# Kernel optimization log

Measured on AMD Instinct MI355X. Metric: run time of the kernel, lower is better.

The kernel has to match this reference:

```python
import jax, jax.numpy as jnp
import numpy as np

N_RAYS, N_SAMPLES, RES = 4096, 256, 128
RGB_C = 15
XYZ_MIN, XYZ_MAX = -1.0, 1.0
NEAR, FAR, STEPSIZE, BG = 0.2, 3.0, 0.5, 1.0
ALPHA_INIT = 0.01
ACT_SHIFT = float(np.log(1.0 / (1.0 - ALPHA_INIT) - 1.0))
N_FREQ = 6
EMB_DIM = 3 + 3 * 2 * N_FREQ  # 39
DIM0 = RGB_C + EMB_DIM        # 54


def _trilinear(grid, u):
    # grid: [C, R, R, R]; u: [N, 3] normalized to [0,1]; align_corners=True
    R = grid.shape[1]
    pos = jnp.clip(u, 0.0, 1.0) * (R - 1)
    i0 = jnp.clip(jnp.floor(pos).astype(jnp.int32), 0, R - 2)
    f = pos - i0.astype(pos.dtype)
    i1 = i0 + 1
    x0, y0, z0 = i0[:, 0], i0[:, 1], i0[:, 2]
    x1, y1, z1 = i1[:, 0], i1[:, 1], i1[:, 2]
    fx, fy, fz = f[:, 0], f[:, 1], f[:, 2]
    c = (grid[:, x0, y0, z0] * ((1 - fx) * (1 - fy) * (1 - fz))
         + grid[:, x1, y0, z0] * (fx * (1 - fy) * (1 - fz))
         + grid[:, x0, y1, z0] * ((1 - fx) * fy * (1 - fz))
         + grid[:, x0, y0, z1] * ((1 - fx) * (1 - fy) * fz)
         + grid[:, x1, y1, z0] * (fx * fy * (1 - fz))
         + grid[:, x1, y0, z1] * (fx * (1 - fy) * fz)
         + grid[:, x0, y1, z1] * ((1 - fx) * fy * fz)
         + grid[:, x1, y1, z1] * (fx * fy * fz))
    return c.T  # [N, C]


def _embed(x):
    # NeRF positional encoding, multires=6, include inputs: [..., 3] -> [..., 39]
    freqs = 2.0 ** jnp.arange(N_FREQ, dtype=x.dtype)
    xb = x[..., None, :] * freqs[:, None]  # [..., 6, 3]
    shp = x.shape[:-1]
    return jnp.concatenate([x, jnp.sin(xb).reshape(*shp, -1), jnp.cos(xb).reshape(*shp, -1)], -1)


def setup_inputs() -> dict:
    key = jax.random.key(0)
    ks = jax.random.split(key, 12)
    return {
        "rays_o": jax.random.uniform(ks[0], (N_RAYS, 3), minval=-0.5, maxval=0.5),
        "rays_d": jax.random.normal(ks[1], (N_RAYS, 3)),
        "viewdirs": jax.random.normal(ks[2], (N_RAYS, 3)),
        "latent_grid": jax.random.normal(ks[3], (1 + RGB_C, RES, RES, RES)) * 0.1,
        "normals_grid": jax.random.normal(ks[4], (3, RES, RES, RES)),
        "W0": jax.random.normal(ks[5], (DIM0, 64)) * 0.1, "b0": jnp.zeros((64,)),
        "W1": jax.random.normal(ks[6], (64, 64)) * 0.1, "b1": jnp.zeros((64,)),
        "W2": jax.random.normal(ks[7], (64, 64)) * 0.1, "b2": jnp.zeros((64,)),
        "W3": jax.random.normal(ks[8], (64, 3)) * 0.1, "b3": jnp.zeros((3,)),
    }


def reference(rays_o, rays_d, viewdirs, latent_grid, normals_grid,
              W0, b0, W1, b1, W2, b2, W3, b3):
    rays_d = rays_d / jnp.linalg.norm(rays_d, axis=-1, keepdims=True)
    viewdirs = viewdirs / jnp.linalg.norm(viewdirs, axis=-1, keepdims=True)
    # sample_ray: uniform steps along each ray
    t = jnp.linspace(NEAR, FAR, N_SAMPLES, dtype=rays_o.dtype)
    ray_pts = rays_o[:, None, :] + rays_d[:, None, :] * t[None, :, None]  # [R,S,3]
    inbbox = jnp.all((ray_pts >= XYZ_MIN) & (ray_pts <= XYZ_MAX), -1)      # [R,S]
    u = ((ray_pts - XYZ_MIN) / (XYZ_MAX - XYZ_MIN)).reshape(-1, 3)
    lat = _trilinear(latent_grid, u).reshape(N_RAYS, N_SAMPLES, 1 + RGB_C)
    nrm = _trilinear(normals_grid, u).reshape(N_RAYS, N_SAMPLES, 3)
    nrm = nrm / jnp.maximum(jnp.linalg.norm(nrm, axis=-1, keepdims=True), 1e-12)
    nrm = jnp.where(inbbox[..., None], nrm, 0.0)
    density = lat[..., 0]
    # activate_density: 1 - exp(-softplus(d + shift) * interval), zero outside bbox
    alpha = jnp.where(inbbox, 1.0 - jnp.exp(-jax.nn.softplus(density + ACT_SHIFT) * STEPSIZE), 0.0)
    # cumprod_exclusive transmittance
    alphainv_cum = jnp.concatenate(
        [jnp.ones_like(alpha[..., :1]), jnp.cumprod(jnp.clip(1.0 - alpha, 1e-10, None), -1)], -1)
    weights = alpha * alphainv_cum[..., :-1]
    # reflection directions: 2*(-v.n)*n + v
    vde = jnp.broadcast_to(viewdirs[:, None, :], nrm.shape)
    dot = jnp.sum(-vde * nrm, -1, keepdims=True)
    refdirs = 2.0 * dot * nrm + vde
    feat = jnp.concatenate([jnp.where(inbbox[..., None], lat[..., 1:], 0.0), _embed(refdirs)], -1)
    h = jax.nn.relu(feat @ W0 + b0)
    h = jax.nn.relu(h @ W1 + b1)
    h = jax.nn.relu(h @ W2 + b2)
    rgb = jnp.where(inbbox[..., None], jax.nn.sigmoid(h @ W3 + b3), 0.0)
    rgb_marched = jnp.sum(weights[..., None] * rgb, -2) + alphainv_cum[..., -1:] * BG
    depth = jnp.linalg.norm(rays_o[:, None, :] - ray_pts, axis=-1)
    depth_marched = jnp.sum(weights * depth, -1) + alphainv_cum[..., -1] * FAR
    disp = 1.0 / depth_marched
    acc = weights.sum(-1)
    normals_marched = jnp.sum(weights[..., None] * nrm, -2)
    return rgb_marched, depth_marched, disp, acc, normals_marched, weights, alphainv_cum
```

## Files before the change

### kernel.cpp

```cpp
#include <hip/hip_runtime.h>
#include <hip/hip_bf16.h>
#include <math.h>

typedef __hip_bfloat16 bf16;
typedef float f32x4 __attribute__((ext_vector_type(4)));
typedef float f32x2 __attribute__((ext_vector_type(2)));
typedef short short8 __attribute__((ext_vector_type(8)));
typedef short short4v __attribute__((ext_vector_type(4)));

#define NRAYS 4096
#define NSAMP 256
#define RESG  128
#define RS2   16384
#define RS3   2097152
#define ACT_SHIFT (-4.59511985013459f)

#define OFLAG 0
#define OBIAS 16
#define ORO   272
#define ORD   12560
#define OVD   24848
#define FRAG_BYTE_OFF 148544
#define LATIL_BYTE_OFF 1048576ULL
#define NRMIL_BYTE_OFF 68157440ULL
#define WS_NEED        101711872ULL

__device__ __forceinline__ float ldT(const float* p, size_t i){ return p[i]; }
__device__ __forceinline__ float ldT(const bf16*  p, size_t i){ return __bfloat162float(p[i]); }

__device__ __forceinline__ unsigned short f2bu(float f){
  unsigned int x = __float_as_uint(f);
  unsigned int r = (x + 0x7FFFu + ((x >> 16) & 1u)) >> 16;
  return (unsigned short)r;
}
__device__ __forceinline__ float bu2f(short s){
  return __uint_as_float(((unsigned int)(unsigned short)s) << 16);
}

#define PREP_BLOCKS 53

template<typename T>
__device__ void fill_ws_part(const void* W0,const void* b0,const void* W1,const void* b1,
                             const void* W2,const void* b2,const void* W3,const void* b3,
                             const void* ro,const void* rd,const void* vd,
                             float* __restrict__ wb, int bid, int tid, bool isf32)
{
  const T* tW0=(const T*)W0; const T* tb0=(const T*)b0;
  const T* tW1=(const T*)W1; const T* tb1=(const T*)b1;
  const T* tW2=(const T*)W2; const T* tb2=(const T*)b2;
  const T* tW3=(const T*)W3; const T* tb3=(const T*)b3;
  const T* tro=(const T*)ro; const T* trd=(const T*)rd; const T* tvd=(const T*)vd;

  unsigned short* fu = (unsigned short*)((char*)wb + FRAG_BYTE_OFF);

  if (bid < 16){
    const int r = bid*256 + tid;
    float ox = ldT(tro, r*3+0), oy = ldT(tro, r*3+1), oz = ldT(tro, r*3+2);
    wb[ORO+r*3+0]=ox; wb[ORO+r*3+1]=oy; wb[ORO+r*3+2]=oz;
    float dx = ldT(trd, r*3+0), dy = ldT(trd, r*3+1), dz = ldT(trd, r*3+2);
    float dn = 1.0f / sqrtf(dx*dx+dy*dy+dz*dz);
    wb[ORD+r*3+0]=dx*dn; wb[ORD+r*3+1]=dy*dn; wb[ORD+r*3+2]=dz*dn;
    float vx = ldT(tvd, r*3+0), vy = ldT(tvd, r*3+1), vz = ldT(tvd, r*3+2);
    float vn = 1.0f / sqrtf(vx*vx+vy*vy+vz*vz);
    wb[OVD+r*3+0]=vx*vn; wb[OVD+r*3+1]=vy*vn; wb[OVD+r*3+2]=vz*vn;
  } else if (bid < 32){
    const int idx = (bid-16)*256 + tid;
    int blk = idx >> 9, rem = idx & 511, lane = rem >> 3, j = rem & 7;
    int nt = blk >> 1, ks = blk & 1;
    int k = ks*32 + ((lane>>4)<<3) + j, n = nt*16 + (lane & 15);
    float v = (k < 54) ? ldT(tW0, k*64 + n) : 0.0f;
    fu[idx] = f2bu(v);
  } else if (bid < 48){
    const int idx = (bid-32)*256 + tid;
    int blk = idx >> 9, rem = idx & 511, lane = rem >> 3, j = rem & 7;
    int nt = blk >> 1, ks = blk & 1;
    int k = ks*32 + ((lane>>4)<<3) + j, n = nt*16 + (lane & 15);
    fu[4096+idx] = f2bu(ldT(tW1, k*64 + n));
    fu[8192+idx] = f2bu(ldT(tW2, k*64 + n));
  } else if (bid < 52){
    const int idx = (bid-48)*256 + tid;
    int blk = idx >> 9, rem = idx & 511, lane = rem >> 3, j = rem & 7;
    int ks = blk;
    int k = ks*32 + ((lane>>4)<<3) + j, n = lane & 15;
    float v = (n < 3) ? ldT(tW3, k*3 + n) : 0.0f;
    fu[12288+idx] = f2bu(v);
  } else {
    if (tid < 64){
      wb[16+tid]  = ldT(tb0, tid);
      wb[80+tid]  = ldT(tb1, tid);
      wb[144+tid] = ldT(tb2, tid);
    }
    if (tid < 16) wb[224+tid] = (tid < 3) ? ldT(tb3, tid) : 0.0f;
    if (tid == 0) wb[OFLAG] = isf32 ? 1.0f : 0.0f;
  }
}

__global__ __launch_bounds__(256)
void prep(const void* W0,const void* b0,const void* W1,const void* b1,
          const void* W2,const void* b2,const void* W3,const void* b3,
          const void* ro,const void* rd,const void* vd,
          float* __restrict__ wb)
{
  __shared__ int s_f32;
  const int tid = threadIdx.x;
  const int bid = blockIdx.x;
  if (tid == 0) s_f32 = 0;
  __syncthreads();
  {
    const bf16* t1 = (const bf16*)W1;
    float a = fabsf(__bfloat162float(t1[2*tid]));
    float b = fabsf(__bfloat162float(t1[2*tid+1]));
    if (!(a < 100.0f) || !(b < 100.0f)) atomicOr(&s_f32, 1);
  }
  __syncthreads();
  const bool isf32 = (s_f32 != 0);
  if (isf32) fill_ws_part<float>(W0,b0,W1,b1,W2,b2,W3,b3,ro,rd,vd,wb,bid,tid,true);
  else       fill_ws_part<bf16 >(W0,b0,W1,b1,W2,b2,W3,b3,ro,rd,vd,wb,bid,tid,false);
}

#define IL_BLOCKS 6144

__global__ __launch_bounds__(256)
void interleave_all(const void* __restrict__ latent, const void* __restrict__ normals,
                    float* __restrict__ wb)
{
  const bool isf32 = (wb[OFLAG] > 0.5f);
  const int bid = blockIdx.x;
  if (bid < 4096){
    unsigned short* lat_il = (unsigned short*)((char*)wb + LATIL_BYTE_OFF);
    const int v0 = (bid*256 + (int)threadIdx.x) * 2;
    short8 o0a, o0b, o1a, o1b;
    if (isf32){
      const float* p = (const float*)latent;
#pragma unroll
      for (int c = 0; c < 8; c++){
        f32x2 r0 = *(const f32x2*)&p[(size_t)c*RS3 + v0];
        o0a[c] = (short)f2bu(r0[0]); o1a[c] = (short)f2bu(r0[1]);
        f32x2 r1 = *(const f32x2*)&p[(size_t)(c+8)*RS3 + v0];
        o0b[c] = (short)f2bu(r1[0]); o1b[c] = (short)f2bu(r1[1]);
      }
    } else {
      const unsigned short* p = (const unsigned short*)latent;
#pragma unroll
      for (int c = 0; c < 8; c++){
        unsigned int r0 = *(const unsigned int*)&p[(size_t)c*RS3 + v0];
        o0a[c] = (short)(r0 & 0xFFFFu); o1a[c] = (short)(r0 >> 16);
        unsigned int r1 = *(const unsigned int*)&p[(size_t)(c+8)*RS3 + v0];
        o0b[c] = (short)(r1 & 0xFFFFu); o1b[c] = (short)(r1 >> 16);
      }
    }
    unsigned short* q = &lat_il[(size_t)v0 << 4];
    *(short8*)&q[0]  = o0a;
    *(short8*)&q[8]  = o0b;
    *(short8*)&q[16] = o1a;
    *(short8*)&q[24] = o1b;
  } else {
    f32x4* nrm_il = (f32x4*)((char*)wb + NRMIL_BYTE_OFF);
    const int v0 = ((bid-4096)*256 + (int)threadIdx.x) * 4;
    f32x4 a, b, c;
    if (isf32){
      const float* p = (const float*)normals;
      a = *(const f32x4*)&p[v0];
      b = *(const f32x4*)&p[(size_t)RS3 + v0];
      c = *(const f32x4*)&p[(size_t)2*RS3 + v0];
    } else {
      const unsigned short* p = (const unsigned short*)normals;
      short4v sa = *(const short4v*)&p[v0];
      short4v sb = *(const short4v*)&p[(size_t)RS3 + v0];
      short4v sc = *(const short4v*)&p[(size_t)2*RS3 + v0];
      a = (f32x4){bu2f(sa[0]), bu2f(sa[1]), bu2f(sa[2]), bu2f(sa[3])};
      b = (f32x4){bu2f(sb[0]), bu2f(sb[1]), bu2f(sb[2]), bu2f(sb[3])};
      c = (f32x4){bu2f(sc[0]), bu2f(sc[1]), bu2f(sc[2]), bu2f(sc[3])};
    }
#pragma unroll
    for (int j = 0; j < 4; j++){
      nrm_il[v0 + j] = (f32x4){a[j], b[j], c[j], 0.0f};
    }
  }
}

__global__ __launch_bounds__(256, 4)
void render_fast(const float* __restrict__ wb, float* __restrict__ out)
{
  const int ray  = blockIdx.x;
  const int i    = threadIdx.x;
  const int lane = i & 63;
  const int wv   = i >> 6;
  const int quad = lane >> 4;
  const int n15  = lane & 15;
  const int wbase = wv * 64;

  __shared__ unsigned short act[NSAMP*72];
  __shared__ float sh_w[NSAMP];
  __shared__ float sh_wt[4];
  __shared__ float red[4][8];
  __shared__ float red_rgb[4][16];

  const unsigned short* lat_il = (const unsigned short*)((const char*)wb + LATIL_BYTE_OFF);
  const f32x4* nrm_il = (const f32x4*)((const char*)wb + NRMIL_BYTE_OFF);

  const float ox = wb[ORO+ray*3+0], oy = wb[ORO+ray*3+1], oz = wb[ORO+ray*3+2];
  const float dx = wb[ORD+ray*3+0], dy = wb[ORD+ray*3+1], dz = wb[ORD+ray*3+2];
  const float vx = wb[OVD+ray*3+0], vy = wb[OVD+ray*3+1], vz = wb[OVD+ray*3+2];

  const float t  = 0.2f + (2.8f/255.0f) * (float)i;
  const float px = ox + dx*t, py = oy + dy*t, pz = oz + dz*t;
  const bool inb = (px >= -1.0f) & (px <= 1.0f) & (py >= -1.0f) & (py <= 1.0f)
                 & (pz >= -1.0f) & (pz <= 1.0f);

  float alpha = 0.0f, nx = 0.0f, ny = 0.0f, nz = 0.0f;
  unsigned short* arow = &act[i*72];

  if (inb) {
    float ux = fminf(fmaxf((px+1.0f)*0.5f, 0.0f), 1.0f) * 127.0f;
    float uy = fminf(fmaxf((py+1.0f)*0.5f, 0.0f), 1.0f) * 127.0f;
    float uz = fminf(fmaxf((pz+1.0f)*0.5f, 0.0f), 1.0f) * 127.0f;
    int x0 = (int)floorf(ux); x0 = x0 > 126 ? 126 : (x0 < 0 ? 0 : x0);
    int y0 = (int)floorf(uy); y0 = y0 > 126 ? 126 : (y0 < 0 ? 0 : y0);
    int z0 = (int)floorf(uz); z0 = z0 > 126 ? 126 : (z0 < 0 ? 0 : z0);
    float fx = ux - (float)x0, fy = uy - (float)y0, fz = uz - (float)z0;
    const float gx = 1.0f - fx, gy = 1.0f - fy, gz = 1.0f - fz;

    const int vb = (x0<<14) + (y0<<7) + z0;
    const unsigned short* Lp = lat_il + ((size_t)vb<<4);
    const f32x4* Np = nrm_il + vb;

    float ch[16];
#pragma unroll
    for (int c = 0; c < 16; c++) ch[c] = 0.0f;
    float nr0 = 0.0f, nr1 = 0.0f, nr2 = 0.0f;

    const int   loff[4] = {0, 1<<18, 1<<11, (1<<18)+(1<<11)};
    const int   noff[4] = {0, 16384, 128, 16384+128};
    const float wxy[4]  = {gx*gy, fx*gy, gx*fy, fx*fy};

#pragma unroll
    for (int cr = 0; cr < 4; cr++){
      const unsigned short* p = Lp + loff[cr];
      short8 a0 = *(const short8*)(p);
      short8 a1 = *(const short8*)(p+8);
      short8 b0 = *(const short8*)(p+16);
      short8 b1 = *(const short8*)(p+24);
      const float wz0 = wxy[cr]*gz, wz1 = wxy[cr]*fz;
#pragma unroll
      for (int j = 0; j < 8; j++){
        ch[j]   += wz0*bu2f(a0[j]) + wz1*bu2f(b0[j]);
        ch[j+8] += wz0*bu2f(a1[j]) + wz1*bu2f(b1[j]);
      }
      f32x4 n0 = Np[noff[cr]];
      f32x4 n1 = Np[noff[cr]+1];
      nr0 += wz0*n0[0] + wz1*n1[0];
      nr1 += wz0*n0[1] + wz1*n1[1];
      nr2 += wz0*n0[2] + wz1*n1[2];
    }

    float xs = ch[0] + ACT_SHIFT;
    float sp = xs > 15.0f ? xs : log1pf(__expf(xs));
    alpha = 1.0f - __expf(-sp * 0.5f);

    float nn  = sqrtf(nr0*nr0 + nr1*nr1 + nr2*nr2);
    float ninv = 1.0f / fmaxf(nn, 1e-12f);
    nx = nr0*ninv; ny = nr1*ninv; nz = nr2*ninv;

    float dt = -(vx*nx + vy*ny + vz*nz);
    float rx = 2.0f*dt*nx + vx, ry = 2.0f*dt*ny + vy, rz = 2.0f*dt*nz + vz;

    short8 v0, v1;
#pragma unroll
    for (int j = 0; j < 8; j++) v0[j] = (short)f2bu(ch[1+j]);
#pragma unroll
    for (int j = 0; j < 7; j++) v1[j] = (short)f2bu(ch[9+j]);
    v1[7] = (short)f2bu(rx);
    *(short8*)&arow[0] = v0; *(short8*)&arow[8] = v1;
    v0[0]=(short)f2bu(ry); v0[1]=(short)f2bu(rz);
    v0[2]=(short)f2bu(__sinf(rx));        v0[3]=(short)f2bu(__sinf(ry));        v0[4]=(short)f2bu(__sinf(rz));
    v0[5]=(short)f2bu(__sinf(rx*2.0f));   v0[6]=(short)f2bu(__sinf(ry*2.0f));   v0[7]=(short)f2bu(__sinf(rz*2.0f));
    v1[0]=(short)f2bu(__sinf(rx*4.0f));   v1[1]=(short)f2bu(__sinf(ry*4.0f));   v1[2]=(short)f2bu(__sinf(rz*4.0f));
    v1[3]=(short)f2bu(__sinf(rx*8.0f));   v1[4]=(short)f2bu(__sinf(ry*8.0f));   v1[5]=(short)f2bu(__sinf(rz*8.0f));
    v1[6]=(short)f2bu(__sinf(rx*16.0f));  v1[7]=(short)f2bu(__sinf(ry*16.0f));
    *(short8*)&arow[16] = v0; *(short8*)&arow[24] = v1;
    v0[0]=(short)f2bu(__sinf(rz*16.0f));  v0[1]=(short)f2bu(__sinf(rx*32.0f));
    v0[2]=(short)f2bu(__sinf(ry*32.0f));  v0[3]=(short)f2bu(__sinf(rz*32.0f));
    v0[4]=(short)f2bu(__cosf(rx));        v0[5]=(short)f2bu(__cosf(ry));        v0[6]=(short)f2bu(__cosf(rz));
    v0[7]=(short)f2bu(__cosf(rx*2.0f));
    v1[0]=(short)f2bu(__cosf(ry*2.0f));   v1[1]=(short)f2bu(__cosf(rz*2.0f));
    v1[2]=(short)f2bu(__cosf(rx*4.0f));   v1[3]=(short)f2bu(__cosf(ry*4.0f));   v1[4]=(short)f2bu(__cosf(rz*4.0f));
    v1[5]=(short)f2bu(__cosf(rx*8.0f));   v1[6]=(short)f2bu(__cosf(ry*8.0f));   v1[7]=(short)f2bu(__cosf(rz*8.0f));
    *(short8*)&arow[32] = v0; *(short8*)&arow[40] = v1;
    v0[0]=(short)f2bu(__cosf(rx*16.0f));  v0[1]=(short)f2bu(__cosf(ry*16.0f));  v0[2]=(short)f2bu(__cosf(rz*16.0f));
    v0[3]=(short)f2bu(__cosf(rx*32.0f));  v0[4]=(short)f2bu(__cosf(ry*32.0f));  v0[5]=(short)f2bu(__cosf(rz*32.0f));
    v0[6]=0; v0[7]=0;
#pragma unroll
    for (int j = 0; j < 8; j++) v1[j] = 0;
    *(short8*)&arow[48] = v0; *(short8*)&arow[56] = v1;
  } else {
    short8 z;
#pragma unroll
    for (int j = 0; j < 8; j++) z[j] = 0;
#pragma unroll
    for (int c = 0; c < 8; c++) *(short8*)&arow[c*8] = z;
  }

  float xv = fmaxf(1.0f - alpha, 1e-10f);
  float incl = xv;
#pragma unroll
  for (int off = 1; off < 64; off <<= 1){
    float y = __shfl_up(incl, off, 64);
    if (lane >= off) incl *= y;
  }
  float excl = __shfl_up(incl, 1, 64);
  if (lane == 0) excl = 1.0f;
  if (lane == 63) sh_wt[wv] = incl;
  __syncthreads();

  float pre = 1.0f;
#pragma unroll
  for (int k = 0; k < 4; k++) if (k < wv) pre *= sh_wt[k];
  const float last = sh_wt[0]*sh_wt[1]*sh_wt[2]*sh_wt[3];
  const float av = pre * excl;
  const float w  = alpha * av;
  sh_w[i] = w;

  float* outw = out + 36864;
  float* outa = out + 36864 + 1048576;
  outw[ray*NSAMP + i] = w;
  outa[ray*(NSAMP+1) + i] = av;
  if (i == NSAMP-1) outa[ray*(NSAMP+1) + NSAMP] = last;

  {
    float vals[5] = { w*t, w, w*nx, w*ny, w*nz };
#pragma unroll
    for (int v = 0; v < 5; v++){
      float s = vals[v];
#pragma unroll
      for (int m = 32; m > 0; m >>= 1) s += __shfl_xor(s, m, 64);
      if (lane == 0) red[wv][v] = s;
    }
  }
  __syncthreads();
  if (i == 0){
    float s0 = red[0][0]+red[1][0]+red[2][0]+red[3][0];
    float s1 = red[0][1]+red[1][1]+red[2][1]+red[3][1];
    float s2 = red[0][2]+red[1][2]+red[2][2]+red[3][2];
    float s3 = red[0][3]+red[1][3]+red[2][3]+red[3][3];
    float s4 = red[0][4]+red[1][4]+red[2][4]+red[3][4];
    const float dm = s0 + last * 3.0f;
    float* o1 = out + 12288; o1[ray] = dm;
    float* o2 = out + 16384; o2[ray] = 1.0f / dm;
    float* o3 = out + 20480; o3[ray] = s1;
    float* o4 = out + 24576;
    o4[ray*3+0] = s2; o4[ray*3+1] = s3; o4[ray*3+2] = s4;
  }

  const short8* fr = (const short8*)((const char*)wb + FRAG_BYTE_OFF);

#pragma unroll
  for (int l = 0; l < 3; l++){
    const int fbase = l * 512;
    f32x4 acc[4][4];
#pragma unroll
    for (int mt = 0; mt < 4; mt++)
#pragma unroll
      for (int nt = 0; nt < 4; nt++) acc[mt][nt] = (f32x4){0.f,0.f,0.f,0.f};

#pragma unroll
    for (int ks = 0; ks < 2; ks++){
      short8 a[4], b[4];
#pragma unroll
      for (int mt = 0; mt < 4; mt++)
        a[mt] = *(const short8*)&act[(wbase + mt*16 + n15)*72 + ks*32 + quad*8];
#pragma unroll
      for (int nt = 0; nt < 4; nt++)
        b[nt] = fr[fbase + (nt*2+ks)*64 + lane];
#pragma unroll
      for (int mt = 0; mt < 4; mt++)
#pragma unroll
        for (int nt = 0; nt < 4; nt++)
          acc[mt][nt] = __builtin_amdgcn_mfma_f32_16x16x32_bf16(a[mt], b[nt], acc[mt][nt], 0, 0, 0);
    }
    __syncthreads();
#pragma unroll
    for (int nt = 0; nt < 4; nt++){
      const float bn = wb[OBIAS + l*64 + nt*16 + n15];
#pragma unroll
      for (int mt = 0; mt < 4; mt++){
#pragma unroll
        for (int r = 0; r < 4; r++){
          float vv = fmaxf(acc[mt][nt][r] + bn, 0.0f);
          act[(wbase + mt*16 + quad*4 + r)*72 + nt*16 + n15] = f2bu(vv);
        }
      }
    }
    __syncthreads();
  }

  {
    f32x4 acc3[4];
#pragma unroll
    for (int mt = 0; mt < 4; mt++) acc3[mt] = (f32x4){0.f,0.f,0.f,0.f};
#pragma unroll
    for (int ks = 0; ks < 2; ks++){
      short8 a[4];
#pragma unroll
      for (int mt = 0; mt < 4; mt++)
        a[mt] = *(const short8*)&act[(wbase + mt*16 + n15)*72 + ks*32 + quad*8];
      short8 b = fr[1536 + ks*64 + lane];
#pragma unroll
      for (int mt = 0; mt < 4; mt++)
        acc3[mt] = __builtin_amdgcn_mfma_f32_16x16x32_bf16(a[mt], b, acc3[mt], 0, 0, 0);
    }
    const float bn3 = wb[OBIAS + 208 + n15];
    float p = 0.0f;
#pragma unroll
    for (int mt = 0; mt < 4; mt++){
#pragma unroll
      for (int r = 0; r < 4; r++){
        const float wr = sh_w[wbase + mt*16 + quad*4 + r];
        const float logit = acc3[mt][r] + bn3;
        p += wr * (1.0f / (1.0f + __expf(-logit)));
      }
    }
    p += __shfl_xor(p, 16, 64);
    p += __shfl_xor(p, 32, 64);
    if (lane < 16) red_rgb[wv][lane] = p;
  }
  __syncthreads();
  if (i < 3){
    float s = red_rgb[0][i] + red_rgb[1][i] + red_rgb[2][i] + red_rgb[3][i];
    out[ray*3+i] = s + last;
  }
}

template<typename GT>
__device__ __forceinline__ void render_body(const GT* __restrict__ latent,
                                            const GT* __restrict__ normals,
                                            const float* __restrict__ wb,
                                            float* __restrict__ out)
{
  const int ray  = blockIdx.x;
  const int i    = threadIdx.x;
  const int lane = i & 63;
  const int wv   = i >> 6;
  const int quad = lane >> 4;
  const int n15  = lane & 15;
  const int wbase = wv * 64;

  __shared__ unsigned short act[NSAMP*72];
  __shared__ float sh_w[NSAMP];
  __shared__ float sh_wt[4];
  __shared__ float red[4][8];
  __shared__ float red_rgb[4][16];

  const float ox = wb[ORO+ray*3+0], oy = wb[ORO+ray*3+1], oz = wb[ORO+ray*3+2];
  const float dx = wb[ORD+ray*3+0], dy = wb[ORD+ray*3+1], dz = wb[ORD+ray*3+2];
  const float vx = wb[OVD+ray*3+0], vy = wb[OVD+ray*3+1], vz = wb[OVD+ray*3+2];

  const float t  = 0.2f + (2.8f/255.0f) * (float)i;
  const float px = ox + dx*t, py = oy + dy*t, pz = oz + dz*t;
  const bool inb = (px >= -1.0f) & (px <= 1.0f) & (py >= -1.0f) & (py <= 1.0f)
                 & (pz >= -1.0f) & (pz <= 1.0f);

  float alpha = 0.0f, nx = 0.0f, ny = 0.0f, nz = 0.0f;
  float fv[64];
#pragma unroll
  for (int k = 0; k < 64; k++) fv[k] = 0.0f;

  if (inb) {
    float ux = fminf(fmaxf((px+1.0f)*0.5f, 0.0f), 1.0f) * 127.0f;
    float uy = fminf(fmaxf((py+1.0f)*0.5f, 0.0f), 1.0f) * 127.0f;
    float uz = fminf(fmaxf((pz+1.0f)*0.5f, 0.0f), 1.0f) * 127.0f;
    int x0 = (int)floorf(ux); x0 = x0 > 126 ? 126 : (x0 < 0 ? 0 : x0);
    int y0 = (int)floorf(uy); y0 = y0 > 126 ? 126 : (y0 < 0 ? 0 : y0);
    int z0 = (int)floorf(uz); z0 = z0 > 126 ? 126 : (z0 < 0 ? 0 : z0);
    float fx = ux - (float)x0, fy = uy - (float)y0, fz = uz - (float)z0;
    const int base = x0*RS2 + y0*RESG + z0;
    const float gx = 1.0f - fx, gy = 1.0f - fy, gz = 1.0f - fz;
    const float w000 = gx*gy*gz, w100 = fx*gy*gz, w010 = gx*fy*gz, w001 = gx*gy*fz;
    const float w110 = fx*fy*gz, w101 = fx*gy*fz, w011 = gx*fy*fz, w111 = fx*fy*fz;

    float ch[19];
#pragma unroll
    for (int c = 0; c < 19; c++){
      const GT* g = (c < 16 ? latent + c*RS3 : normals + (c-16)*RS3) + base;
      ch[c] = w000*ldT(g,0)        + w100*ldT(g,RS2)
            + w010*ldT(g,RESG)     + w001*ldT(g,1)
            + w110*ldT(g,RS2+RESG) + w101*ldT(g,RS2+1)
            + w011*ldT(g,RESG+1)   + w111*ldT(g,RS2+RESG+1);
    }

    float xs = ch[0] + ACT_SHIFT;
    float sp = xs > 15.0f ? xs : log1pf(__expf(xs));
    alpha = 1.0f - __expf(-sp * 0.5f);

    float nn  = sqrtf(ch[16]*ch[16] + ch[17]*ch[17] + ch[18]*ch[18]);
    float ninv = 1.0f / fmaxf(nn, 1e-12f);
    nx = ch[16]*ninv; ny = ch[17]*ninv; nz = ch[18]*ninv;

    float dt = -(vx*nx + vy*ny + vz*nz);
    float rx = 2.0f*dt*nx + vx, ry = 2.0f*dt*ny + vy, rz = 2.0f*dt*nz + vz;

#pragma unroll
    for (int k = 0; k < 15; k++) fv[k] = ch[k+1];
    fv[15] = rx; fv[16] = ry; fv[17] = rz;
#pragma unroll
    for (int f = 0; f < 6; f++){
      float s = (float)(1 << f);
      fv[18 + f*3 + 0] = __sinf(rx*s);
      fv[18 + f*3 + 1] = __sinf(ry*s);
      fv[18 + f*3 + 2] = __sinf(rz*s);
      fv[36 + f*3 + 0] = __cosf(rx*s);
      fv[36 + f*3 + 1] = __cosf(ry*s);
      fv[36 + f*3 + 2] = __cosf(rz*s);
    }
  }

#pragma unroll
  for (int c = 0; c < 8; c++){
    short8 v;
#pragma unroll
    for (int k = 0; k < 8; k++) v[k] = (short)f2bu(fv[c*8+k]);
    *(short8*)&act[i*72 + c*8] = v;
  }

  float xvv = fmaxf(1.0f - alpha, 1e-10f);
  float incl = xvv;
#pragma unroll
  for (int off = 1; off < 64; off <<= 1){
    float y = __shfl_up(incl, off, 64);
    if (lane >= off) incl *= y;
  }
  float excl = __shfl_up(incl, 1, 64);
  if (lane == 0) excl = 1.0f;
  if (lane == 63) sh_wt[wv] = incl;
  __syncthreads();

  float pre = 1.0f;
#pragma unroll
  for (int k = 0; k < 4; k++) if (k < wv) pre *= sh_wt[k];
  const float last = sh_wt[0]*sh_wt[1]*sh_wt[2]*sh_wt[3];
  const float av = pre * excl;
  const float w  = alpha * av;
  sh_w[i] = w;

  float* outw = out + 36864;
  float* outa = out + 36864 + 1048576;
  outw[ray*NSAMP + i] = w;
  outa[ray*(NSAMP+1) + i] = av;
  if (i == NSAMP-1) outa[ray*(NSAMP+1) + NSAMP] = last;

  {
    float vals[5] = { w*t, w, w*nx, w*ny, w*nz };
#pragma unroll
    for (int v = 0; v < 5; v++){
      float s = vals[v];
#pragma unroll
      for (int m = 32; m > 0; m >>= 1) s += __shfl_xor(s, m, 64);
      if (lane == 0) red[wv][v] = s;
    }
  }
  __syncthreads();
  if (i == 0){
    float s0 = red[0][0]+red[1][0]+red[2][0]+red[3][0];
    float s1 = red[0][1]+red[1][1]+red[2][1]+red[3][1];
    float s2 = red[0][2]+red[1][2]+red[2][2]+red[3][2];
    float s3 = red[0][3]+red[1][3]+red[2][3]+red[3][3];
    float s4 = red[0][4]+red[1][4]+red[2][4]+red[3][4];
    const float dm = s0 + last * 3.0f;
    float* o1 = out + 12288; o1[ray] = dm;
    float* o2 = out + 16384; o2[ray] = 1.0f / dm;
    float* o3 = out + 20480; o3[ray] = s1;
    float* o4 = out + 24576;
    o4[ray*3+0] = s2; o4[ray*3+1] = s3; o4[ray*3+2] = s4;
  }

  const short8* fr = (const short8*)((const char*)wb + FRAG_BYTE_OFF);

#pragma unroll
  for (int l = 0; l < 3; l++){
    const int fbase = l * 512;
    f32x4 acc[4][4];
#pragma unroll
    for (int mt = 0; mt < 4; mt++)
#pragma unroll
      for (int nt = 0; nt < 4; nt++) acc[mt][nt] = (f32x4){0.f,0.f,0.f,0.f};

#pragma unroll
    for (int ks = 0; ks < 2; ks++){
      short8 a[4], b[4];
#pragma unroll
      for (int mt = 0; mt < 4; mt++)
        a[mt] = *(const short8*)&act[(wbase + mt*16 + n15)*72 + ks*32 + quad*8];
#pragma unroll
      for (int nt = 0; nt < 4; nt++)
        b[nt] = fr[fbase + (nt*2+ks)*64 + lane];
#pragma unroll
      for (int mt = 0; mt < 4; mt++)
#pragma unroll
        for (int nt = 0; nt < 4; nt++)
          acc[mt][nt] = __builtin_amdgcn_mfma_f32_16x16x32_bf16(a[mt], b[nt], acc[mt][nt], 0, 0, 0);
    }
    __syncthreads();
#pragma unroll
    for (int nt = 0; nt < 4; nt++){
      const float bn = wb[OBIAS + l*64 + nt*16 + n15];
#pragma unroll
      for (int mt = 0; mt < 4; mt++){
#pragma unroll
        for (int r = 0; r < 4; r++){
          float vv = fmaxf(acc[mt][nt][r] + bn, 0.0f);
          act[(wbase + mt*16 + quad*4 + r)*72 + nt*16 + n15] = f2bu(vv);
        }
      }
    }
    __syncthreads();
  }

  {
    f32x4 acc3[4];
#pragma unroll
    for (int mt = 0; mt < 4; mt++) acc3[mt] = (f32x4){0.f,0.f,0.f,0.f};
#pragma unroll
    for (int ks = 0; ks < 2; ks++){
      short8 a[4];
#pragma unroll
      for (int mt = 0; mt < 4; mt++)
        a[mt] = *(const short8*)&act[(wbase + mt*16 + n15)*72 + ks*32 + quad*8];
      short8 b = fr[1536 + ks*64 + lane];
#pragma unroll
      for (int mt = 0; mt < 4; mt++)
        acc3[mt] = __builtin_amdgcn_mfma_f32_16x16x32_bf16(a[mt], b, acc3[mt], 0, 0, 0);
    }
    const float bn3 = wb[OBIAS + 208 + n15];
    float p = 0.0f;
#pragma unroll
    for (int mt = 0; mt < 4; mt++){
#pragma unroll
      for (int r = 0; r < 4; r++){
        const float wr = sh_w[wbase + mt*16 + quad*4 + r];
        const float logit = acc3[mt][r] + bn3;
        p += wr * (1.0f / (1.0f + __expf(-logit)));
      }
    }
    p += __shfl_xor(p, 16, 64);
    p += __shfl_xor(p, 32, 64);
    if (lane < 16) red_rgb[wv][lane] = p;
  }
  __syncthreads();
  if (i < 3){
    float s = red_rgb[0][i] + red_rgb[1][i] + red_rgb[2][i] + red_rgb[3][i];
    out[ray*3+i] = s + last;
  }
}

__global__ __launch_bounds__(256)
void render_fallback(const void* __restrict__ latent, const void* __restrict__ normals,
                     const float* __restrict__ wb, float* __restrict__ out)
{
  if (wb[OFLAG] > 0.5f)
    render_body<float>((const float*)latent, (const float*)normals, wb, out);
  else
    render_body<bf16 >((const bf16*)latent,  (const bf16*)normals,  wb, out);
}

extern "C" void kernel_launch(void* const* d_in, const int* in_sizes, int n_in,
                              void* d_out, int out_size, void* d_ws, size_t ws_size,
                              hipStream_t stream)
{
  float* wb = (float*)d_ws;
  prep<<<PREP_BLOCKS, 256, 0, stream>>>(d_in[5], d_in[6], d_in[7], d_in[8],
                                        d_in[9], d_in[10], d_in[11], d_in[12],
                                        d_in[0], d_in[1], d_in[2], wb);
  if (ws_size >= WS_NEED){
    interleave_all<<<IL_BLOCKS, 256, 0, stream>>>(d_in[3], d_in[4], wb);
    render_fast<<<NRAYS, 256, 0, stream>>>(wb, (float*)d_out);
  } else {
    render_fallback<<<NRAYS, 256, 0, stream>>>(d_in[3], d_in[4], wb, (float*)d_out);
  }
}
```

Before: 347.2 us.

## Merge prep and interleave kernels; use packed bf16 converts and sincos

Folds the weight-prep kernel and the grid interleave kernel into one launch. Each block works out the dtype flag locally, so the interleave no longer has to wait on a flag written by an earlier kernel. Float-to-bf16 conversion now uses the v_cvt_pk_bf16_f32 instruction, which converts two values per instruction, in place of manual rounding bit-math. The positional-encoding sin and cos pairs are computed with __sincosf. This removes one kernel launch and cuts ALU work in the per-sample feature build, at the cost of inline asm tied to this GPU architecture and of every block repeating the W1 dtype check.

```diff
diff --git a/kernel.cpp b/kernel.cpp
--- a/kernel.cpp
+++ b/kernel.cpp
@@ -36,6 +36,12 @@
 __device__ __forceinline__ float bu2f(short s){
   return __uint_as_float(((unsigned int)(unsigned short)s) << 16);
 }
+__device__ __forceinline__ unsigned int pkbf(float lo, float hi){
+  unsigned int r;
+  asm("v_cvt_pk_bf16_f32 %0, %1, %2" : "=v"(r) : "v"(lo), "v"(hi));
+  return r;
+}
+union SU { short8 s; unsigned int u[4]; };
 
 #define PREP_BLOCKS 53
 
@@ -95,11 +101,14 @@
   }
 }
 
+#define STAGE_BLOCKS 6208
+
 __global__ __launch_bounds__(256)
-void prep(const void* W0,const void* b0,const void* W1,const void* b1,
-          const void* W2,const void* b2,const void* W3,const void* b3,
-          const void* ro,const void* rd,const void* vd,
-          float* __restrict__ wb)
+void stage(const void* W0,const void* b0,const void* W1,const void* b1,
+           const void* W2,const void* b2,const void* W3,const void* b3,
+           const void* ro,const void* rd,const void* vd,
+           const void* __restrict__ latent, const void* __restrict__ normals,
+           float* __restrict__ wb)
 {
   __shared__ int s_f32;
   const int tid = threadIdx.x;
@@ -114,49 +123,47 @@
   }
   __syncthreads();
   const bool isf32 = (s_f32 != 0);
-  if (isf32) fill_ws_part<float>(W0,b0,W1,b1,W2,b2,W3,b3,ro,rd,vd,wb,bid,tid,true);
-  else       fill_ws_part<bf16 >(W0,b0,W1,b1,W2,b2,W3,b3,ro,rd,vd,wb,bid,tid,false);
-}
-
-#define IL_BLOCKS 6144
-
-__global__ __launch_bounds__(256)
-void interleave_all(const void* __restrict__ latent, const void* __restrict__ normals,
-                    float* __restrict__ wb)
-{
-  const bool isf32 = (wb[OFLAG] > 0.5f);
-  const int bid = blockIdx.x;
-  if (bid < 4096){
+
+  if (bid < 64){
+    if (bid < PREP_BLOCKS){
+      if (isf32) fill_ws_part<float>(W0,b0,W1,b1,W2,b2,W3,b3,ro,rd,vd,wb,bid,tid,true);
+      else       fill_ws_part<bf16 >(W0,b0,W1,b1,W2,b2,W3,b3,ro,rd,vd,wb,bid,tid,false);
+    }
+  } else if (bid < 64 + 4096){
     unsigned short* lat_il = (unsigned short*)((char*)wb + LATIL_BYTE_OFF);
-    const int v0 = (bid*256 + (int)threadIdx.x) * 2;
-    short8 o0a, o0b, o1a, o1b;
+    const int v0 = ((bid-64)*256 + tid) * 2;
+    SU o0a, o0b, o1a, o1b;
     if (isf32){
       const float* p = (const float*)latent;
 #pragma unroll
-      for (int c = 0; c < 8; c++){
-        f32x2 r0 = *(const f32x2*)&p[(size_t)c*RS3 + v0];
-        o0a[c] = (short)f2bu(r0[0]); o1a[c] = (short)f2bu(r0[1]);
-        f32x2 r1 = *(const f32x2*)&p[(size_t)(c+8)*RS3 + v0];
-        o0b[c] = (short)f2bu(r1[0]); o1b[c] = (short)f2bu(r1[1]);
+      for (int c = 0; c < 4; c++){
+        f32x2 ra = *(const f32x2*)&p[(size_t)(2*c  )*RS3 + v0];
+        f32x2 rb = *(const f32x2*)&p[(size_t)(2*c+1)*RS3 + v0];
+        o0a.u[c] = pkbf(ra[0], rb[0]);
+        o1a.u[c] = pkbf(ra[1], rb[1]);
+        f32x2 rc = *(const f32x2*)&p[(size_t)(2*c+8)*RS3 + v0];
+        f32x2 rd2= *(const f32x2*)&p[(size_t)(2*c+9)*RS3 + v0];
+        o0b.u[c] = pkbf(rc[0], rd2[0]);
+        o1b.u[c] = pkbf(rc[1], rd2[1]);
       }
     } else {
       const unsigned short* p = (const unsigned short*)latent;
 #pragma unroll
       for (int c = 0; c < 8; c++){
         unsigned int r0 = *(const unsigned int*)&p[(size_t)c*RS3 + v0];
-        o0a[c] = (short)(r0 & 0xFFFFu); o1a[c] = (short)(r0 >> 16);
+        o0a.s[c] = (short)(r0 & 0xFFFFu); o1a.s[c] = (short)(r0 >> 16);
         unsigned int r1 = *(const unsigned int*)&p[(size_t)(c+8)*RS3 + v0];
-        o0b[c] = (short)(r1 & 0xFFFFu); o1b[c] = (short)(r1 >> 16);
+        o0b.s[c] = (short)(r1 & 0xFFFFu); o1b.s[c] = (short)(r1 >> 16);
       }
     }
     unsigned short* q = &lat_il[(size_t)v0 << 4];
-    *(short8*)&q[0]  = o0a;
-    *(short8*)&q[8]  = o0b;
-    *(short8*)&q[16] = o1a;
-    *(short8*)&q[24] = o1b;
+    *(short8*)&q[0]  = o0a.s;
+    *(short8*)&q[8]  = o0b.s;
+    *(short8*)&q[16] = o1a.s;
+    *(short8*)&q[24] = o1b.s;
   } else {
     f32x4* nrm_il = (f32x4*)((char*)wb + NRMIL_BYTE_OFF);
-    const int v0 = ((bid-4096)*256 + (int)threadIdx.x) * 4;
+    const int v0 = ((bid-4160)*256 + tid) * 4;
     f32x4 a, b, c;
     if (isf32){
       const float* p = (const float*)normals;
@@ -179,6 +186,29 @@
   }
 }
 
+__global__ __launch_bounds__(256)
+void prep(const void* W0,const void* b0,const void* W1,const void* b1,
+          const void* W2,const void* b2,const void* W3,const void* b3,
+          const void* ro,const void* rd,const void* vd,
+          float* __restrict__ wb)
+{
+  __shared__ int s_f32;
+  const int tid = threadIdx.x;
+  const int bid = blockIdx.x;
+  if (tid == 0) s_f32 = 0;
+  __syncthreads();
+  {
+    const bf16* t1 = (const bf16*)W1;
+    float a = fabsf(__bfloat162float(t1[2*tid]));
+    float b = fabsf(__bfloat162float(t1[2*tid+1]));
+    if (!(a < 100.0f) || !(b < 100.0f)) atomicOr(&s_f32, 1);
+  }
+  __syncthreads();
+  const bool isf32 = (s_f32 != 0);
+  if (isf32) fill_ws_part<float>(W0,b0,W1,b1,W2,b2,W3,b3,ro,rd,vd,wb,bid,tid,true);
+  else       fill_ws_part<bf16 >(W0,b0,W1,b1,W2,b2,W3,b3,ro,rd,vd,wb,bid,tid,false);
+}
+
 __global__ __launch_bounds__(256, 4)
 void render_fast(const float* __restrict__ wb, float* __restrict__ out)
 {
@@ -265,34 +295,35 @@
     float dt = -(vx*nx + vy*ny + vz*nz);
     float rx = 2.0f*dt*nx + vx, ry = 2.0f*dt*ny + vy, rz = 2.0f*dt*nz + vz;
 
-    short8 v0, v1;
-#pragma unroll
-    for (int j = 0; j < 8; j++) v0[j] = (short)f2bu(ch[1+j]);
-#pragma unroll
-    for (int j = 0; j < 7; j++) v1[j] = (short)f2bu(ch[9+j]);
-    v1[7] = (short)f2bu(rx);
-    *(short8*)&arow[0] = v0; *(short8*)&arow[8] = v1;
-    v0[0]=(short)f2bu(ry); v0[1]=(short)f2bu(rz);
-    v0[2]=(short)f2bu(__sinf(rx));        v0[3]=(short)f2bu(__sinf(ry));        v0[4]=(short)f2bu(__sinf(rz));
-    v0[5]=(short)f2bu(__sinf(rx*2.0f));   v0[6]=(short)f2bu(__sinf(ry*2.0f));   v0[7]=(short)f2bu(__sinf(rz*2.0f));
-    v1[0]=(short)f2bu(__sinf(rx*4.0f));   v1[1]=(short)f2bu(__sinf(ry*4.0f));   v1[2]=(short)f2bu(__sinf(rz*4.0f));
-    v1[3]=(short)f2bu(__sinf(rx*8.0f));   v1[4]=(short)f2bu(__sinf(ry*8.0f));   v1[5]=(short)f2bu(__sinf(rz*8.0f));
-    v1[6]=(short)f2bu(__sinf(rx*16.0f));  v1[7]=(short)f2bu(__sinf(ry*16.0f));
-    *(short8*)&arow[16] = v0; *(short8*)&arow[24] = v1;
-    v0[0]=(short)f2bu(__sinf(rz*16.0f));  v0[1]=(short)f2bu(__sinf(rx*32.0f));
-    v0[2]=(short)f2bu(__sinf(ry*32.0f));  v0[3]=(short)f2bu(__sinf(rz*32.0f));
-    v0[4]=(short)f2bu(__cosf(rx));        v0[5]=(short)f2bu(__cosf(ry));        v0[6]=(short)f2bu(__cosf(rz));
-    v0[7]=(short)f2bu(__cosf(rx*2.0f));
-    v1[0]=(short)f2bu(__cosf(ry*2.0f));   v1[1]=(short)f2bu(__cosf(rz*2.0f));
-    v1[2]=(short)f2bu(__cosf(rx*4.0f));   v1[3]=(short)f2bu(__cosf(ry*4.0f));   v1[4]=(short)f2bu(__cosf(rz*4.0f));
-    v1[5]=(short)f2bu(__cosf(rx*8.0f));   v1[6]=(short)f2bu(__cosf(ry*8.0f));   v1[7]=(short)f2bu(__cosf(rz*8.0f));
-    *(short8*)&arow[32] = v0; *(short8*)&arow[40] = v1;
-    v0[0]=(short)f2bu(__cosf(rx*16.0f));  v0[1]=(short)f2bu(__cosf(ry*16.0f));  v0[2]=(short)f2bu(__cosf(rz*16.0f));
-    v0[3]=(short)f2bu(__cosf(rx*32.0f));  v0[4]=(short)f2bu(__cosf(ry*32.0f));  v0[5]=(short)f2bu(__cosf(rz*32.0f));
-    v0[6]=0; v0[7]=0;
-#pragma unroll
-    for (int j = 0; j < 8; j++) v1[j] = 0;
-    *(short8*)&arow[48] = v0; *(short8*)&arow[56] = v1;
+    float sX[6], sY[6], sZ[6], cX[6], cY[6], cZ[6];
+#pragma unroll
+    for (int f = 0; f < 6; f++){
+      const float s = (float)(1 << f);
+      __sincosf(rx*s, &sX[f], &cX[f]);
+      __sincosf(ry*s, &sY[f], &cY[f]);
+      __sincosf(rz*s, &sZ[f], &cZ[f]);
+    }
+
+    SU v0, v1;
+    v0.u[0]=pkbf(ch[1],ch[2]);   v0.u[1]=pkbf(ch[3],ch[4]);
+    v0.u[2]=pkbf(ch[5],ch[6]);   v0.u[3]=pkbf(ch[7],ch[8]);
+    v1.u[0]=pkbf(ch[9],ch[10]);  v1.u[1]=pkbf(ch[11],ch[12]);
+    v1.u[2]=pkbf(ch[13],ch[14]); v1.u[3]=pkbf(ch[15],rx);
+    *(short8*)&arow[0] = v0.s; *(short8*)&arow[8] = v1.s;
+    v0.u[0]=pkbf(ry,rz);         v0.u[1]=pkbf(sX[0],sY[0]);
+    v0.u[2]=pkbf(sZ[0],sX[1]);   v0.u[3]=pkbf(sY[1],sZ[1]);
+    v1.u[0]=pkbf(sX[2],sY[2]);   v1.u[1]=pkbf(sZ[2],sX[3]);
+    v1.u[2]=pkbf(sY[3],sZ[3]);   v1.u[3]=pkbf(sX[4],sY[4]);
+    *(short8*)&arow[16] = v0.s; *(short8*)&arow[24] = v1.s;
+    v0.u[0]=pkbf(sZ[4],sX[5]);   v0.u[1]=pkbf(sY[5],sZ[5]);
+    v0.u[2]=pkbf(cX[0],cY[0]);   v0.u[3]=pkbf(cZ[0],cX[1]);
+    v1.u[0]=pkbf(cY[1],cZ[1]);   v1.u[1]=pkbf(cX[2],cY[2]);
+    v1.u[2]=pkbf(cZ[2],cX[3]);   v1.u[3]=pkbf(cY[3],cZ[3]);
+    *(short8*)&arow[32] = v0.s; *(short8*)&arow[40] = v1.s;
+    v0.u[0]=pkbf(cX[4],cY[4]);   v0.u[1]=pkbf(cZ[4],cX[5]);
+    v0.u[2]=pkbf(cY[5],cZ[5]);   v0.u[3]=0u;
+    v1.u[0]=0u; v1.u[1]=0u; v1.u[2]=0u; v1.u[3]=0u;
+    *(short8*)&arow[48] = v0.s; *(short8*)&arow[56] = v1.s;
   } else {
     short8 z;
 #pragma unroll
@@ -387,7 +418,7 @@
 #pragma unroll
         for (int r = 0; r < 4; r++){
           float vv = fmaxf(acc[mt][nt][r] + bn, 0.0f);
-          act[(wbase + mt*16 + quad*4 + r)*72 + nt*16 + n15] = f2bu(vv);
+          act[(wbase + mt*16 + quad*4 + r)*72 + nt*16 + n15] = (unsigned short)pkbf(vv, vv);
         }
       }
     }
@@ -667,13 +698,16 @@
                               hipStream_t stream)
 {
   float* wb = (float*)d_ws;
-  prep<<<PREP_BLOCKS, 256, 0, stream>>>(d_in[5], d_in[6], d_in[7], d_in[8],
-                                        d_in[9], d_in[10], d_in[11], d_in[12],
-                                        d_in[0], d_in[1], d_in[2], wb);
   if (ws_size >= WS_NEED){
-    interleave_all<<<IL_BLOCKS, 256, 0, stream>>>(d_in[3], d_in[4], wb);
+    stage<<<STAGE_BLOCKS, 256, 0, stream>>>(d_in[5], d_in[6], d_in[7], d_in[8],
+                                            d_in[9], d_in[10], d_in[11], d_in[12],
+                                            d_in[0], d_in[1], d_in[2],
+                                            d_in[3], d_in[4], wb);
     render_fast<<<NRAYS, 256, 0, stream>>>(wb, (float*)d_out);
   } else {
+    prep<<<PREP_BLOCKS, 256, 0, stream>>>(d_in[5], d_in[6], d_in[7], d_in[8],
+                                          d_in[9], d_in[10], d_in[11], d_in[12],
+                                          d_in[0], d_in[1], d_in[2], wb);
     render_fallback<<<NRAYS, 256, 0, stream>>>(d_in[3], d_in[4], wb, (float*)d_out);
   }
 }
```

Measured after the change: 334.2 us. -3.7%, faster.
